# Kernel tuning notes

Measured on AMD Instinct MI355X. Metric: run time of the kernel, lower is better.

Reference implementation:

```python
import jax, jax.numpy as jnp
import numpy as np

N_LAYER = 4
N_HEAD = 12
D_MODEL = 768
SEQ_LEN = 2048
VOCAB = 50257
BATCH = 2


def _sinusoid_pe(seq_len, d_model):
    pos = np.arange(seq_len, dtype=np.float32)[:, None]
    div = np.exp(np.arange(0, d_model, 2, dtype=np.float32) * (-np.log(10000.0) / d_model))
    pe = np.zeros((seq_len, d_model), dtype=np.float32)
    pe[:, 0::2] = np.sin(pos * div)
    pe[:, 1::2] = np.cos(pos * div)
    return jnp.asarray(pe[None])  # [1, C, D]


def setup_inputs() -> dict:
    key = jax.random.key(0)
    ks = jax.random.split(key, 12)
    s = 0.02
    return {
        "features": jax.random.randint(ks[0], (BATCH, SEQ_LEN), 0, VOCAB),
        "targets": jax.random.randint(ks[1], (BATCH, SEQ_LEN), 0, VOCAB),
        "tok_embed": jax.random.normal(ks[2], (VOCAB, D_MODEL), jnp.float32) * s,
        "pos_emb": _sinusoid_pe(SEQ_LEN, D_MODEL),
        "ln1_w": jnp.ones((N_LAYER, D_MODEL), jnp.float32),
        "ln1_b": jnp.zeros((N_LAYER, D_MODEL), jnp.float32),
        "attn_w": jax.random.normal(ks[3], (N_LAYER, D_MODEL, 3 * D_MODEL), jnp.float32) * s,
        "attn_b": jnp.zeros((N_LAYER, 3 * D_MODEL), jnp.float32),
        "proj_w": jax.random.normal(ks[4], (N_LAYER, D_MODEL, D_MODEL), jnp.float32) * s,
        "proj_b": jnp.zeros((N_LAYER, D_MODEL), jnp.float32),
        "ln2_w": jnp.ones((N_LAYER, D_MODEL), jnp.float32),
        "ln2_b": jnp.zeros((N_LAYER, D_MODEL), jnp.float32),
        "ffn_w1": jax.random.normal(ks[5], (N_LAYER, D_MODEL, 4 * D_MODEL), jnp.float32) * s,
        "ffn_b1": jnp.zeros((N_LAYER, 4 * D_MODEL), jnp.float32),
        "ffn_w2": jax.random.normal(ks[6], (N_LAYER, 4 * D_MODEL, D_MODEL), jnp.float32) * s,
        "ffn_b2": jnp.zeros((N_LAYER, D_MODEL), jnp.float32),
        "lnf_w": jnp.ones((D_MODEL,), jnp.float32),
        "lnf_b": jnp.zeros((D_MODEL,), jnp.float32),
        "final_w": jax.random.normal(ks[7], (D_MODEL, VOCAB), jnp.float32) * s,
    }


def _layernorm(x, w, b, eps=1e-5):
    mu = jnp.mean(x, axis=-1, keepdims=True)
    var = jnp.var(x, axis=-1, keepdims=True)
    return (x - mu) * jax.lax.rsqrt(var + eps) * w + b


def _attention(x, wqkv, bqkv, wo, bo):
    B, C, E = x.shape
    dh = E // N_HEAD
    qkv = x @ wqkv + bqkv  # [B, C, 3E]
    q, k, v = jnp.split(qkv, 3, axis=-1)
    q = q.reshape(B, C, N_HEAD, dh)
    k = k.reshape(B, C, N_HEAD, dh)
    v = v.reshape(B, C, N_HEAD, dh)
    att = jnp.einsum("bqhd,bkhd->bhqk", q, k) / jnp.sqrt(jnp.float32(dh))
    causal = jnp.tril(jnp.ones((C, C), bool))
    att = jnp.where(causal, att, -jnp.inf)
    att = jax.nn.softmax(att, axis=-1)
    y = jnp.einsum("bhqk,bkhd->bqhd", att, v).reshape(B, C, E)
    return y @ wo + bo


def reference(features, targets, tok_embed, pos_emb, ln1_w, ln1_b, attn_w, attn_b,
              proj_w, proj_b, ln2_w, ln2_b, ffn_w1, ffn_b1, ffn_w2, ffn_b2,
              lnf_w, lnf_b, final_w):
    C = features.shape[1]
    x = tok_embed[features] + pos_emb[:, :C]
    for l in range(N_LAYER):
        h = _layernorm(x, ln1_w[l], ln1_b[l])
        x = x + _attention(h, attn_w[l], attn_b[l], proj_w[l], proj_b[l])
        h = _layernorm(x, ln2_w[l], ln2_b[l])
        h = jax.nn.gelu(h @ ffn_w1[l] + ffn_b1[l], approximate=False) @ ffn_w2[l] + ffn_b2[l]
        x = x + h
    x = _layernorm(x, lnf_w, lnf_b)
    logits = x @ final_w  # [B, C, V]
    logp = jax.nn.log_softmax(logits, axis=-1)
    tgt = targets.reshape(-1)
    valid = tgt != -1
    tgt_safe = jnp.where(valid, tgt, 0)
    nll = -jnp.take_along_axis(logp.reshape(-1, logits.shape[-1]), tgt_safe[:, None], axis=1)[:, 0]
    loss = jnp.sum(jnp.where(valid, nll, 0.0)) / jnp.maximum(jnp.sum(valid), 1)
    return logits, loss
```

## Files before the change

### kernel.cpp

```cpp
#include <hip/hip_runtime.h>
#include <math.h>

#define N_LAYER 4
#define N_HEAD  12
#define D_MODEL 768
#define SEQ     2048
#define VOCAB   50257
#define BATCH   2
#define MROWS   (BATCH*SEQ)

typedef __bf16 bf16;
typedef __bf16 bf16x8 __attribute__((ext_vector_type(8)));
typedef float  f32x4  __attribute__((ext_vector_type(4)));
typedef short  short8v __attribute__((ext_vector_type(8)));

__device__ __forceinline__ void gload16(const bf16* g, const bf16* l) {
    __builtin_amdgcn_global_load_lds(
        (const __attribute__((address_space(1))) void*)g,
        (__attribute__((address_space(3))) void*)l,
        16, 0, 0);
}

__global__ __launch_bounds__(256) void embed_kernel(
    const int* __restrict__ feat, const float* __restrict__ tok,
    const float* __restrict__ pos, float* __restrict__ x)
{
    int row = blockIdx.x;
    int cpos = row & (SEQ - 1);
    int tid = feat[row];
    const float* te = tok + (size_t)tid * D_MODEL;
    const float* pe = pos + (size_t)cpos * D_MODEL;
    float* xr = x + (size_t)row * D_MODEL;
    for (int c = threadIdx.x; c < D_MODEL; c += 256)
        xr[c] = te[c] + pe[c];
}

__global__ __launch_bounds__(256) void ln_kernel(
    const float* __restrict__ x, const float* __restrict__ w,
    const float* __restrict__ b, bf16* __restrict__ out)
{
    int wid = threadIdx.x >> 6, lane = threadIdx.x & 63;
    int row = blockIdx.x * 4 + wid;
    const float* xr = x + (size_t)row * D_MODEL;
    float lv[12];
    float s = 0.f, ss = 0.f;
#pragma unroll
    for (int i = 0; i < 12; i++) {
        float v = xr[lane + i * 64];
        lv[i] = v; s += v; ss += v * v;
    }
#pragma unroll
    for (int o = 32; o; o >>= 1) { s += __shfl_down(s, o, 64); ss += __shfl_down(ss, o, 64); }
    s = __shfl(s, 0, 64); ss = __shfl(ss, 0, 64);
    float mu  = s * (1.f / D_MODEL);
    float var = ss * (1.f / D_MODEL) - mu * mu;
    float rs  = rsqrtf(var + 1e-5f);
#pragma unroll
    for (int i = 0; i < 12; i++) {
        int c = lane + i * 64;
        out[(size_t)row * D_MODEL + c] = (bf16)((lv[i] - mu) * rs * w[c] + b[c]);
    }
}

__global__ __launch_bounds__(256) void transpose_conv_kernel(
    const float* __restrict__ W, bf16* __restrict__ Wt, int K, int N)
{
    int l = blockIdx.z;
    const float* Wl = W + (size_t)l * K * N;
    bf16* Wtl = Wt + (size_t)l * K * N;
    __shared__ float tile[32][33];
    int k0 = blockIdx.y * 32, n0 = blockIdx.x * 32;
    for (int idx = threadIdx.x; idx < 1024; idx += 256) {
        int i = idx >> 5, j = idx & 31;
        int n = n0 + j;
        tile[i][j] = (n < N) ? Wl[(size_t)(k0 + i) * N + n] : 0.f;
    }
    __syncthreads();
    for (int idx = threadIdx.x; idx < 1024; idx += 256) {
        int j = idx >> 5, i = idx & 31;
        int n = n0 + j;
        if (n < N) Wtl[(size_t)n * K + k0 + i] = (bf16)tile[i][j];
    }
}

template<bool BIAS, bool GELU_, int OUTM, int SPLITK>
__global__ __launch_bounds__(256) void gemm_kernel(
    const bf16* __restrict__ A, const bf16* __restrict__ Bt,
    const float* __restrict__ bias, void* __restrict__ Cout,
    bf16* __restrict__ vTout,
    int M, int N, int K)
{
    __shared__ __align__(16) bf16 As[2][128 * 32];
    __shared__ __align__(16) bf16 Bs[2][128 * 32];
    int tid = threadIdx.x;
    int lane = tid & 63, wid = tid >> 6;

    int Kslice = K / SPLITK;
    int kbase = (SPLITK > 1) ? (int)blockIdx.z * Kslice : 0;

    int row0 = blockIdx.x * 128;
    int col0 = blockIdx.y * 128;

    int wr = (wid >> 1) * 64, wc = (wid & 1) * 64;

    int srow = wid * 16 + (lane >> 2);
    int selem = (lane & 3) * 8;
    const bf16* Ab0 = A + (size_t)(row0 + srow) * K + kbase + selem;
    const bf16* Ab1 = Ab0 + (size_t)64 * K;
    int bn0 = col0 + srow;      if (bn0 >= N) bn0 = N - 1;
    int bn1 = col0 + srow + 64; if (bn1 >= N) bn1 = N - 1;
    const bf16* Bb0 = Bt + (size_t)bn0 * K + kbase + selem;
    const bf16* Bb1 = Bt + (size_t)bn1 * K + kbase + selem;

    const int nt = Kslice >> 5;
    int fr = lane & 15, fg8 = (lane >> 4) * 8;

    auto stage = [&](int t, int b) {
        int k0 = t * 32;
        gload16(Ab0 + k0, As[b] + wid * 512);
        gload16(Ab1 + k0, As[b] + (wid + 4) * 512);
        gload16(Bb0 + k0, Bs[b] + wid * 512);
        gload16(Bb1 + k0, Bs[b] + (wid + 4) * 512);
    };

    f32x4 acc[4][4] = {};
    stage(0, 0);

    for (int t = 0; t < nt; ++t) {
        int cur = t & 1;
        if (t + 1 < nt) {
            stage(t + 1, cur ^ 1);
            asm volatile("s_waitcnt vmcnt(4)" ::: "memory");
        } else {
            asm volatile("s_waitcnt vmcnt(0)" ::: "memory");
        }
        __builtin_amdgcn_s_barrier();

        bf16x8 af[4], bfr[4];
#pragma unroll
        for (int m = 0; m < 4; m++) af[m] = *(const bf16x8*)&As[cur][(wr + m * 16 + fr) * 32 + fg8];
#pragma unroll
        for (int n = 0; n < 4; n++) bfr[n] = *(const bf16x8*)&Bs[cur][(wc + n * 16 + fr) * 32 + fg8];
#pragma unroll
        for (int m = 0; m < 4; m++)
#pragma unroll
            for (int n = 0; n < 4; n++)
                acc[m][n] = __builtin_amdgcn_mfma_f32_16x16x32_bf16(af[m], bfr[n], acc[m][n], 0, 0, 0);

        asm volatile("s_waitcnt lgkmcnt(0)" ::: "memory");
        __builtin_amdgcn_s_barrier();
    }

    int g = lane >> 4;
    bool addbias = BIAS && (SPLITK == 1 || blockIdx.z == 0);

#pragma unroll
    for (int m = 0; m < 4; m++) {
#pragma unroll
        for (int n = 0; n < 4; n++) {
            int col = col0 + wc + n * 16 + fr;
            bool ok = (col < N);
            float bv = (addbias && ok) ? bias[col] : 0.f;
#pragma unroll
            for (int r = 0; r < 4; r++) {
                int row = row0 + wr + m * 16 + g * 4 + r;
                float v = acc[m][n][r] + bv;
                if (GELU_) v = 0.5f * v * (1.f + erff(v * 0.70710678118f));
                if (ok) {
                    if (OUTM == 1)
                        ((bf16*)Cout)[(size_t)row * N + col] = (bf16)v;
                    else if (OUTM == 3) {
                        if (col < 2 * D_MODEL) {
                            ((bf16*)Cout)[(size_t)row * N + col] = (bf16)v;
                        } else {
                            int c2 = col - 2 * D_MODEL;
                            int hh = c2 >> 6, dd = c2 & 63;
                            int bb = row >> 11, ss = row & (SEQ - 1);
                            vTout[(((size_t)(bb * N_HEAD + hh) * 64 + dd) << 11) + ss] = (bf16)v;
                        }
                    }
                    else if (SPLITK > 1)
                        atomicAdd(&((float*)Cout)[(size_t)row * N + col], v);
                    else
                        ((float*)Cout)[(size_t)row * N + col] += v;
                }
            }
        }
    }
}

__global__ __launch_bounds__(512, 2) void gemm256_logits_kernel(
    const bf16* __restrict__ A, const bf16* __restrict__ Bt,
    float* __restrict__ Cout, float* __restrict__ rowsum, int N, int K)
{
    __shared__ __align__(16) bf16 As[2][256 * 64];
    __shared__ __align__(16) bf16 Bs[2][256 * 64];
    int tid = threadIdx.x, lane = tid & 63, wid = tid >> 6;
    int wm = wid >> 2, wn = wid & 3;
    int row0 = blockIdx.x * 256, col0 = blockIdx.y * 256;
    int fr = lane & 15, fg8 = (lane >> 4) * 8, g = lane >> 4;

    int srow_c = lane >> 3;
    int scol   = ((lane & 7) ^ srow_c) * 8;
    int sw     = (fr & 7) << 3;
    int cswz0  = (0 * 32 + fg8) ^ sw;
    int cswz1  = (1 * 32 + fg8) ^ sw;

    const int nt = K >> 6;

    auto stageA = [&](int t, int half) {
        int buf = t & 1, k0 = t * 64;
#pragma unroll
        for (int j = 0; j < 2; j++) {
            int rloc = half * 128 + (wid * 2 + j) * 8;
            gload16(A + (size_t)(row0 + rloc + srow_c) * K + k0 + scol,
                    As[buf] + rloc * 64);
        }
    };
    auto stageB = [&](int t, int half) {
        int buf = t & 1, k0 = t * 64;
#pragma unroll
        for (int j = 0; j < 2; j++) {
            int rloc = half * 128 + (wid * 2 + j) * 8;
            int grow = col0 + rloc + srow_c;
            if (grow >= N) grow = N - 1;
            gload16(Bt + (size_t)grow * K + k0 + scol,
                    Bs[buf] + rloc * 64);
        }
    };

    f32x4 acc[8][4] = {};

    stageA(0, 0); stageA(0, 1); stageB(0, 0); stageB(0, 1);
    stageB(1, 0); stageB(1, 1);
    asm volatile("s_waitcnt vmcnt(4)" ::: "memory");
    __builtin_amdgcn_s_barrier();

    for (int t = 0; t < nt; ++t) {
        int c = t & 1;
        const bf16* Ac = As[c];
        const bf16* Bc = Bs[c];

        bf16x8 bfrag[4][2];
#pragma unroll
        for (int n = 0; n < 4; n++) {
            bfrag[n][0] = *(const bf16x8*)&Bc[(wn * 64 + n * 16 + fr) * 64 + cswz0];
            bfrag[n][1] = *(const bf16x8*)&Bc[(wn * 64 + n * 16 + fr) * 64 + cswz1];
        }
        {
            bf16x8 a_[2][2];
#pragma unroll
            for (int mi = 0; mi < 2; mi++) {
                a_[mi][0] = *(const bf16x8*)&Ac[(wm * 128 + mi * 16 + fr) * 64 + cswz0];
                a_[mi][1] = *(const bf16x8*)&Ac[(wm * 128 + mi * 16 + fr) * 64 + cswz1];
            }
            if (t + 1 < nt) stageA(t + 1, 0);
            __builtin_amdgcn_s_barrier();
            __builtin_amdgcn_s_setprio(1);
#pragma unroll
            for (int mi = 0; mi < 2; mi++)
#pragma unroll
                for (int n = 0; n < 4; n++)
#pragma unroll
                    for (int ks = 0; ks < 2; ks++)
                        acc[mi][n] = __builtin_amdgcn_mfma_f32_16x16x32_bf16(a_[mi][ks], bfrag[n][ks], acc[mi][n], 0, 0, 0);
            __builtin_amdgcn_s_setprio(0);
            __builtin_amdgcn_s_barrier();
        }
        {
            bf16x8 a_[2][2];
#pragma unroll
            for (int mi = 0; mi < 2; mi++) {
                a_[mi][0] = *(const bf16x8*)&Ac[(wm * 128 + (2 + mi) * 16 + fr) * 64 + cswz0];
                a_[mi][1] = *(const bf16x8*)&Ac[(wm * 128 + (2 + mi) * 16 + fr) * 64 + cswz1];
            }
            if (t + 1 < nt) stageA(t + 1, 1);
            if (t + 2 < nt) stageB(t + 2, 0);
            __builtin_amdgcn_s_barrier();
            __builtin_amdgcn_s_setprio(1);
#pragma unroll
            for (int mi = 0; mi < 2; mi++)
#pragma unroll
                for (int n = 0; n < 4; n++)
#pragma unroll
                    for (int ks = 0; ks < 2; ks++)
                        acc[2 + mi][n] = __builtin_amdgcn_mfma_f32_16x16x32_bf16(a_[mi][ks], bfrag[n][ks], acc[2 + mi][n], 0, 0, 0);
            __builtin_amdgcn_s_setprio(0);
            __builtin_amdgcn_s_barrier();
        }
        {
            bf16x8 a_[2][2];
#pragma unroll
            for (int mi = 0; mi < 2; mi++) {
                a_[mi][0] = *(const bf16x8*)&Ac[(wm * 128 + (4 + mi) * 16 + fr) * 64 + cswz0];
                a_[mi][1] = *(const bf16x8*)&Ac[(wm * 128 + (4 + mi) * 16 + fr) * 64 + cswz1];
            }
            if (t + 2 < nt) stageB(t + 2, 1);
            __builtin_amdgcn_s_barrier();
            __builtin_amdgcn_s_setprio(1);
#pragma unroll
            for (int mi = 0; mi < 2; mi++)
#pragma unroll
                for (int n = 0; n < 4; n++)
#pragma unroll
                    for (int ks = 0; ks < 2; ks++)
                        acc[4 + mi][n] = __builtin_amdgcn_mfma_f32_16x16x32_bf16(a_[mi][ks], bfrag[n][ks], acc[4 + mi][n], 0, 0, 0);
            __builtin_amdgcn_s_setprio(0);
            __builtin_amdgcn_s_barrier();
        }
        {
            bf16x8 a_[2][2];
#pragma unroll
            for (int mi = 0; mi < 2; mi++) {
                a_[mi][0] = *(const bf16x8*)&Ac[(wm * 128 + (6 + mi) * 16 + fr) * 64 + cswz0];
                a_[mi][1] = *(const bf16x8*)&Ac[(wm * 128 + (6 + mi) * 16 + fr) * 64 + cswz1];
            }
            __builtin_amdgcn_s_barrier();
            __builtin_amdgcn_s_setprio(1);
#pragma unroll
            for (int mi = 0; mi < 2; mi++)
#pragma unroll
                for (int n = 0; n < 4; n++)
#pragma unroll
                    for (int ks = 0; ks < 2; ks++)
                        acc[6 + mi][n] = __builtin_amdgcn_mfma_f32_16x16x32_bf16(a_[mi][ks], bfrag[n][ks], acc[6 + mi][n], 0, 0, 0);
            __builtin_amdgcn_s_setprio(0);
            if (t + 2 < nt)
                asm volatile("s_waitcnt vmcnt(4)" ::: "memory");
            else if (t + 1 < nt)
                asm volatile("s_waitcnt vmcnt(0)" ::: "memory");
            __builtin_amdgcn_s_barrier();
        }
    }

#pragma unroll
    for (int mf = 0; mf < 8; mf++) {
        float lsum[4] = {0.f, 0.f, 0.f, 0.f};
#pragma unroll
        for (int n = 0; n < 4; n++) {
            int col = col0 + wn * 64 + n * 16 + fr;
            bool ok = (col < N);
#pragma unroll
            for (int r = 0; r < 4; r++) {
                int row = row0 + wm * 128 + mf * 16 + g * 4 + r;
                float v = acc[mf][n][r];
                if (ok) {
                    Cout[(size_t)row * N + col] = v;
                    lsum[r] += __expf(v);
                }
            }
        }
#pragma unroll
        for (int r = 0; r < 4; r++) {
            float s = lsum[r];
#pragma unroll
            for (int o = 1; o < 16; o <<= 1) s += __shfl_xor(s, o, 64);
            if (fr == 0)
                atomicAdd(&rowsum[row0 + wm * 128 + mf * 16 + g * 4 + r], s);
        }
    }
}

__global__ __launch_bounds__(256) void attn_kernel(
    const bf16* __restrict__ qkv, const bf16* __restrict__ vT, bf16* __restrict__ y)
{
    int qt = (int)(gridDim.x - 1 - blockIdx.x), h = blockIdx.y, b = blockIdx.z;
    const size_t rs = 3 * D_MODEL;
    int tid = threadIdx.x, lane = tid & 63, wid = tid >> 6;
    int fr = lane & 15, g = lane >> 4;
    int wq = qt * 64 + wid * 16;

    const bf16* qb = qkv + (size_t)b * SEQ * rs + h * 64;
    const bf16* kb = qb + D_MODEL;
    const bf16* vb = vT + ((size_t)(b * N_HEAD + h) * 64) * SEQ;

    __shared__ bf16 Ps[4][16][72];

    bf16x8 aq[2];
#pragma unroll
    for (int kk = 0; kk < 2; kk++)
        aq[kk] = *(const bf16x8*)&qb[(size_t)(wq + fr) * rs + kk * 32 + g * 8];

    f32x4 acco[4] = {};
    float mrow[4], lrow[4];
#pragma unroll
    for (int r = 0; r < 4; r++) { mrow[r] = -1e30f; lrow[r] = 0.f; }

    int jmax = qt * 64;
    for (int j0 = 0; j0 <= jmax; j0 += 64) {
        f32x4 accs[4] = {};
#pragma unroll
        for (int n = 0; n < 4; n++)
#pragma unroll
            for (int kk = 0; kk < 2; kk++) {
                bf16x8 bk = *(const bf16x8*)&kb[(size_t)(j0 + n * 16 + fr) * rs + kk * 32 + g * 8];
                accs[n] = __builtin_amdgcn_mfma_f32_16x16x32_bf16(aq[kk], bk, accs[n], 0, 0, 0);
            }

        bool diag = (j0 == jmax);
#pragma unroll
        for (int n = 0; n < 4; n++) {
            int jc = j0 + n * 16 + fr;
#pragma unroll
            for (int r = 0; r < 4; r++) {
                float sv = accs[n][r] * 0.125f;
                if (diag) { int irow = wq + g * 4 + r; if (jc > irow) sv = -1e30f; }
                accs[n][r] = sv;
            }
        }

        float pscale[4];
#pragma unroll
        for (int r = 0; r < 4; r++) {
            float pm = fmaxf(fmaxf(accs[0][r], accs[1][r]), fmaxf(accs[2][r], accs[3][r]));
#pragma unroll
            for (int o = 1; o < 16; o <<= 1) pm = fmaxf(pm, __shfl_xor(pm, o, 64));
            float mnew = fmaxf(mrow[r], pm);
            float corr = __expf(mrow[r] - mnew);
            mrow[r] = mnew;
            float ls = 0.f;
#pragma unroll
            for (int n = 0; n < 4; n++) {
                float p = __expf(accs[n][r] - mnew);
                accs[n][r] = p; ls += p;
            }
#pragma unroll
            for (int o = 1; o < 16; o <<= 1) ls += __shfl_xor(ls, o, 64);
            lrow[r] = lrow[r] * corr + ls;
            pscale[r] = corr;
        }
#pragma unroll
        for (int n = 0; n < 4; n++)
#pragma unroll
            for (int r = 0; r < 4; r++) acco[n][r] *= pscale[r];

#pragma unroll
        for (int n = 0; n < 4; n++)
#pragma unroll
            for (int r = 0; r < 4; r++)
                Ps[wid][g * 4 + r][n * 16 + fr] = (bf16)accs[n][r];

        bf16x8 ap[2];
#pragma unroll
        for (int kk = 0; kk < 2; kk++)
            ap[kk] = *(const bf16x8*)&Ps[wid][fr][kk * 32 + g * 8];
#pragma unroll
        for (int kk = 0; kk < 2; kk++)
#pragma unroll
            for (int n = 0; n < 4; n++) {
                bf16x8 bv = *(const bf16x8*)&vb[(size_t)(n * 16 + fr) * SEQ + j0 + kk * 32 + g * 8];
                acco[n] = __builtin_amdgcn_mfma_f32_16x16x32_bf16(ap[kk], bv, acco[n], 0, 0, 0);
            }
    }

    bf16* yb = y + (size_t)b * SEQ * D_MODEL + h * 64;
#pragma unroll
    for (int n = 0; n < 4; n++)
#pragma unroll
        for (int r = 0; r < 4; r++) {
            int row = wq + g * 4 + r;
            yb[(size_t)row * D_MODEL + n * 16 + fr] = (bf16)(acco[n][r] / lrow[r]);
        }
}

__global__ __launch_bounds__(256) void loss_nll_kernel(
    const float* __restrict__ logits, const float* __restrict__ rowsum,
    const int* __restrict__ tgt, float* __restrict__ accum)
{
    int row = blockIdx.x * 256 + threadIdx.x;
    if (row >= MROWS) return;
    int t = tgt[row];
    if (t >= 0) {
        float nll = logf(rowsum[row]) - logits[(size_t)row * VOCAB + t];
        atomicAdd(accum, nll);
        atomicAdd(accum + 1, 1.f);
    }
}

__global__ void loss_final_kernel(const float* __restrict__ accum, float* __restrict__ out)
{
    out[0] = accum[0] / fmaxf(accum[1], 1.f);
}

extern "C" void kernel_launch(void* const* d_in, const int* in_sizes, int n_in,
                              void* d_out, int out_size, void* d_ws, size_t ws_size,
                              hipStream_t stream)
{
    const int*   feat  = (const int*)d_in[0];
    const int*   tgt   = (const int*)d_in[1];
    const float* tok   = (const float*)d_in[2];
    const float* pos   = (const float*)d_in[3];
    const float* ln1w  = (const float*)d_in[4];
    const float* ln1b  = (const float*)d_in[5];
    const float* attnw = (const float*)d_in[6];
    const float* attnb = (const float*)d_in[7];
    const float* projw = (const float*)d_in[8];
    const float* projb = (const float*)d_in[9];
    const float* ln2w  = (const float*)d_in[10];
    const float* ln2b  = (const float*)d_in[11];
    const float* fw1   = (const float*)d_in[12];
    const float* fb1   = (const float*)d_in[13];
    const float* fw2   = (const float*)d_in[14];
    const float* fb2   = (const float*)d_in[15];
    const float* lnfw  = (const float*)d_in[16];
    const float* lnfb  = (const float*)d_in[17];
    const float* finw  = (const float*)d_in[18];

    char* ws = (char*)d_ws;
    size_t off = 0;
    auto alloc = [&](size_t bytes) -> void* {
        void* p = ws + off; off += (bytes + 255) & ~(size_t)255; return p;
    };
    float* x     = (float*)alloc((size_t)MROWS * D_MODEL * 4);
    bf16*  h     = (bf16*) alloc((size_t)MROWS * D_MODEL * 2);
    bf16*  big   = (bf16*) alloc((size_t)MROWS * 4 * D_MODEL * 2);
    bf16*  ybuf  = (bf16*) alloc((size_t)MROWS * D_MODEL * 2);
    bf16*  vT    = (bf16*) alloc((size_t)BATCH * N_HEAD * 64 * SEQ * 2);
    bf16*  awt   = (bf16*) alloc((size_t)N_LAYER * 3 * D_MODEL * D_MODEL * 2);
    bf16*  pwt   = (bf16*) alloc((size_t)N_LAYER * D_MODEL * D_MODEL * 2);
    bf16*  f1wt  = (bf16*) alloc((size_t)N_LAYER * 4 * D_MODEL * D_MODEL * 2);
    bf16*  f2wt  = (bf16*) alloc((size_t)N_LAYER * 4 * D_MODEL * D_MODEL * 2);
    bf16*  fwt   = (bf16*) alloc((size_t)VOCAB * D_MODEL * 2);
    float* rowsum= (float*)alloc((size_t)MROWS * 4);
    float* accum = (float*)alloc(256);

    float* logits = (float*)d_out;
    float* lossp  = (float*)d_out + (size_t)MROWS * VOCAB;

    dim3 blk(256);
    transpose_conv_kernel<<<dim3(3 * D_MODEL / 32, D_MODEL / 32, N_LAYER), blk, 0, stream>>>(attnw, awt, D_MODEL, 3 * D_MODEL);
    transpose_conv_kernel<<<dim3(D_MODEL / 32, D_MODEL / 32, N_LAYER), blk, 0, stream>>>(projw, pwt, D_MODEL, D_MODEL);
    transpose_conv_kernel<<<dim3(4 * D_MODEL / 32, D_MODEL / 32, N_LAYER), blk, 0, stream>>>(fw1, f1wt, D_MODEL, 4 * D_MODEL);
    transpose_conv_kernel<<<dim3(D_MODEL / 32, 4 * D_MODEL / 32, N_LAYER), blk, 0, stream>>>(fw2, f2wt, 4 * D_MODEL, D_MODEL);
    transpose_conv_kernel<<<dim3((VOCAB + 31) / 32, D_MODEL / 32, 1), blk, 0, stream>>>(finw, fwt, D_MODEL, VOCAB);

    embed_kernel<<<MROWS, blk, 0, stream>>>(feat, tok, pos, x);

    for (int l = 0; l < N_LAYER; l++) {
        ln_kernel<<<MROWS / 4, blk, 0, stream>>>(x, ln1w + l * D_MODEL, ln1b + l * D_MODEL, h);
        gemm_kernel<true, false, 3, 1><<<dim3(MROWS / 128, (3 * D_MODEL) / 128), blk, 0, stream>>>(
            h, awt + (size_t)l * 3 * D_MODEL * D_MODEL, attnb + l * 3 * D_MODEL, big, vT,
            MROWS, 3 * D_MODEL, D_MODEL);
        attn_kernel<<<dim3(SEQ / 64, N_HEAD, BATCH), blk, 0, stream>>>(big, vT, ybuf);
        gemm_kernel<true, false, 2, 2><<<dim3(MROWS / 128, D_MODEL / 128, 2), blk, 0, stream>>>(
            ybuf, pwt + (size_t)l * D_MODEL * D_MODEL, projb + l * D_MODEL, x, nullptr,
            MROWS, D_MODEL, D_MODEL);
        ln_kernel<<<MROWS / 4, blk, 0, stream>>>(x, ln2w + l * D_MODEL, ln2b + l * D_MODEL, h);
        gemm_kernel<true, true, 1, 1><<<dim3(MROWS / 128, (4 * D_MODEL) / 128), blk, 0, stream>>>(
            h, f1wt + (size_t)l * 4 * D_MODEL * D_MODEL, fb1 + l * 4 * D_MODEL, big, nullptr,
            MROWS, 4 * D_MODEL, D_MODEL);
        gemm_kernel<true, false, 2, 2><<<dim3(MROWS / 128, D_MODEL / 128, 2), blk, 0, stream>>>(
            big, f2wt + (size_t)l * 4 * D_MODEL * D_MODEL, fb2 + l * D_MODEL, x, nullptr,
            MROWS, D_MODEL, 4 * D_MODEL);
    }

    ln_kernel<<<MROWS / 4, blk, 0, stream>>>(x, lnfw, lnfb, h);

    hipMemsetAsync(rowsum, 0, (size_t)MROWS * 4, stream);
    hipMemsetAsync(accum, 0, 8, stream);

    gemm256_logits_kernel<<<dim3(MROWS / 256, (VOCAB + 255) / 256), dim3(512), 0, stream>>>(
        h, fwt, logits, rowsum, VOCAB, D_MODEL);

    loss_nll_kernel<<<(MROWS + 255) / 256, blk, 0, stream>>>(logits, rowsum, tgt, accum);
    loss_final_kernel<<<1, 1, 0, stream>>>(accum, lossp);

    (void)in_sizes; (void)n_in; (void)out_size; (void)ws_size;
}
```

Baseline: 2.069 ms.

## Single-buffer logits GEMM LDS and raise occupancy hint instead of prefetch pipeline

Drops the double-buffered LDS staging and the interleaved prefetch of the next K tile in the 256x256 logits GEMM. Each iteration now loads the tile, waits for all loads, computes, then syncs. This halves shared memory per block, and the launch bound is raised to 4 blocks per CU, betting on more resident blocks to hide latency. The cost is that the in-block overlap between global loads and MFMA is lost, and 4 blocks of 512 threads with 32 f32x4 accumulators each may not fit in the register budget.

```diff
diff --git a/kernel.cpp b/kernel.cpp
--- a/kernel.cpp
+++ b/kernel.cpp
@@ -189,12 +189,12 @@
     }
 }
 
-__global__ __launch_bounds__(512, 2) void gemm256_logits_kernel(
+__global__ __launch_bounds__(512, 4) void gemm256_logits_kernel(
     const bf16* __restrict__ A, const bf16* __restrict__ Bt,
     float* __restrict__ Cout, float* __restrict__ rowsum, int N, int K)
 {
-    __shared__ __align__(16) bf16 As[2][256 * 64];
-    __shared__ __align__(16) bf16 Bs[2][256 * 64];
+    __shared__ __align__(16) bf16 As[256 * 64];
+    __shared__ __align__(16) bf16 Bs[256 * 64];
     int tid = threadIdx.x, lane = tid & 63, wid = tid >> 6;
     int wm = wid >> 2, wn = wid & 3;
     int row0 = blockIdx.x * 256, col0 = blockIdx.y * 256;
@@ -208,129 +208,47 @@
 
     const int nt = K >> 6;
 
-    auto stageA = [&](int t, int half) {
-        int buf = t & 1, k0 = t * 64;
-#pragma unroll
-        for (int j = 0; j < 2; j++) {
-            int rloc = half * 128 + (wid * 2 + j) * 8;
+    auto stage = [&](int t) {
+        int k0 = t * 64;
+#pragma unroll
+        for (int j = 0; j < 4; j++) {
+            int rloc = (wid * 4 + j) * 8;
             gload16(A + (size_t)(row0 + rloc + srow_c) * K + k0 + scol,
-                    As[buf] + rloc * 64);
-        }
-    };
-    auto stageB = [&](int t, int half) {
-        int buf = t & 1, k0 = t * 64;
-#pragma unroll
-        for (int j = 0; j < 2; j++) {
-            int rloc = half * 128 + (wid * 2 + j) * 8;
+                    As + rloc * 64);
             int grow = col0 + rloc + srow_c;
             if (grow >= N) grow = N - 1;
             gload16(Bt + (size_t)grow * K + k0 + scol,
-                    Bs[buf] + rloc * 64);
+                    Bs + rloc * 64);
         }
     };
 
     f32x4 acc[8][4] = {};
 
-    stageA(0, 0); stageA(0, 1); stageB(0, 0); stageB(0, 1);
-    stageB(1, 0); stageB(1, 1);
-    asm volatile("s_waitcnt vmcnt(4)" ::: "memory");
-    __builtin_amdgcn_s_barrier();
-
     for (int t = 0; t < nt; ++t) {
-        int c = t & 1;
-        const bf16* Ac = As[c];
-        const bf16* Bc = Bs[c];
+        stage(t);
+        asm volatile("s_waitcnt vmcnt(0)" ::: "memory");
+        __builtin_amdgcn_s_barrier();
 
         bf16x8 bfrag[4][2];
 #pragma unroll
         for (int n = 0; n < 4; n++) {
-            bfrag[n][0] = *(const bf16x8*)&Bc[(wn * 64 + n * 16 + fr) * 64 + cswz0];
-            bfrag[n][1] = *(const bf16x8*)&Bc[(wn * 64 + n * 16 + fr) * 64 + cswz1];
-        }
-        {
-            bf16x8 a_[2][2];
-#pragma unroll
-            for (int mi = 0; mi < 2; mi++) {
-                a_[mi][0] = *(const bf16x8*)&Ac[(wm * 128 + mi * 16 + fr) * 64 + cswz0];
-                a_[mi][1] = *(const bf16x8*)&Ac[(wm * 128 + mi * 16 + fr) * 64 + cswz1];
-            }
-            if (t + 1 < nt) stageA(t + 1, 0);
-            __builtin_amdgcn_s_barrier();
-            __builtin_amdgcn_s_setprio(1);
-#pragma unroll
-            for (int mi = 0; mi < 2; mi++)
-#pragma unroll
-                for (int n = 0; n < 4; n++)
-#pragma unroll
-                    for (int ks = 0; ks < 2; ks++)
-                        acc[mi][n] = __builtin_amdgcn_mfma_f32_16x16x32_bf16(a_[mi][ks], bfrag[n][ks], acc[mi][n], 0, 0, 0);
-            __builtin_amdgcn_s_setprio(0);
-            __builtin_amdgcn_s_barrier();
-        }
-        {
-            bf16x8 a_[2][2];
-#pragma unroll
-            for (int mi = 0; mi < 2; mi++) {
-                a_[mi][0] = *(const bf16x8*)&Ac[(wm * 128 + (2 + mi) * 16 + fr) * 64 + cswz0];
-                a_[mi][1] = *(const bf16x8*)&Ac[(wm * 128 + (2 + mi) * 16 + fr) * 64 + cswz1];
-            }
-            if (t + 1 < nt) stageA(t + 1, 1);
-            if (t + 2 < nt) stageB(t + 2, 0);
-            __builtin_amdgcn_s_barrier();
-            __builtin_amdgcn_s_setprio(1);
-#pragma unroll
-            for (int mi = 0; mi < 2; mi++)
-#pragma unroll
-                for (int n = 0; n < 4; n++)
-#pragma unroll
-                    for (int ks = 0; ks < 2; ks++)
-                        acc[2 + mi][n] = __builtin_amdgcn_mfma_f32_16x16x32_bf16(a_[mi][ks], bfrag[n][ks], acc[2 + mi][n], 0, 0, 0);
-            __builtin_amdgcn_s_setprio(0);
-            __builtin_amdgcn_s_barrier();
-        }
-        {
-            bf16x8 a_[2][2];
-#pragma unroll
-            for (int mi = 0; mi < 2; mi++) {
-                a_[mi][0] = *(const bf16x8*)&Ac[(wm * 128 + (4 + mi) * 16 + fr) * 64 + cswz0];
-                a_[mi][1] = *(const bf16x8*)&Ac[(wm * 128 + (4 + mi) * 16 + fr) * 64 + cswz1];
-            }
-            if (t + 2 < nt) stageB(t + 2, 1);
-            __builtin_amdgcn_s_barrier();
-            __builtin_amdgcn_s_setprio(1);
-#pragma unroll
-            for (int mi = 0; mi < 2; mi++)
-#pragma unroll
-                for (int n = 0; n < 4; n++)
-#pragma unroll
-                    for (int ks = 0; ks < 2; ks++)
-                        acc[4 + mi][n] = __builtin_amdgcn_mfma_f32_16x16x32_bf16(a_[mi][ks], bfrag[n][ks], acc[4 + mi][n], 0, 0, 0);
-            __builtin_amdgcn_s_setprio(0);
-            __builtin_amdgcn_s_barrier();
-        }
-        {
-            bf16x8 a_[2][2];
-#pragma unroll
-            for (int mi = 0; mi < 2; mi++) {
-                a_[mi][0] = *(const bf16x8*)&Ac[(wm * 128 + (6 + mi) * 16 + fr) * 64 + cswz0];
-                a_[mi][1] = *(const bf16x8*)&Ac[(wm * 128 + (6 + mi) * 16 + fr) * 64 + cswz1];
-            }
-            __builtin_amdgcn_s_barrier();
-            __builtin_amdgcn_s_setprio(1);
-#pragma unroll
-            for (int mi = 0; mi < 2; mi++)
-#pragma unroll
-                for (int n = 0; n < 4; n++)
-#pragma unroll
-                    for (int ks = 0; ks < 2; ks++)
-                        acc[6 + mi][n] = __builtin_amdgcn_mfma_f32_16x16x32_bf16(a_[mi][ks], bfrag[n][ks], acc[6 + mi][n], 0, 0, 0);
-            __builtin_amdgcn_s_setprio(0);
-            if (t + 2 < nt)
-                asm volatile("s_waitcnt vmcnt(4)" ::: "memory");
-            else if (t + 1 < nt)
-                asm volatile("s_waitcnt vmcnt(0)" ::: "memory");
-            __builtin_amdgcn_s_barrier();
-        }
+            bfrag[n][0] = *(const bf16x8*)&Bs[(wn * 64 + n * 16 + fr) * 64 + cswz0];
+            bfrag[n][1] = *(const bf16x8*)&Bs[(wn * 64 + n * 16 + fr) * 64 + cswz1];
+        }
+        __builtin_amdgcn_s_setprio(1);
+#pragma unroll
+        for (int mf = 0; mf < 8; mf++) {
+            bf16x8 a0 = *(const bf16x8*)&As[(wm * 128 + mf * 16 + fr) * 64 + cswz0];
+            bf16x8 a1 = *(const bf16x8*)&As[(wm * 128 + mf * 16 + fr) * 64 + cswz1];
+#pragma unroll
+            for (int n = 0; n < 4; n++) {
+                acc[mf][n] = __builtin_amdgcn_mfma_f32_16x16x32_bf16(a0, bfrag[n][0], acc[mf][n], 0, 0, 0);
+                acc[mf][n] = __builtin_amdgcn_mfma_f32_16x16x32_bf16(a1, bfrag[n][1], acc[mf][n], 0, 0, 0);
+            }
+        }
+        __builtin_amdgcn_s_setprio(0);
+        asm volatile("s_waitcnt lgkmcnt(0)" ::: "memory");
+        __builtin_amdgcn_s_barrier();
     }
 
 #pragma unroll
```

New measurement: 4.989 ms. 141% more time.
